# Performance work log

Measured on AMD Instinct MI355X. Metric: run time of the kernel, lower is better.

The kernel has to match this reference:

```python
import jax, jax.numpy as jnp
import numpy as np

MAX_SHIFT = 15
FREQ_WEIGHT = 0.5
EPS = 1e-8


def setup_inputs() -> dict:
    key = jax.random.key(0)
    k1, k2 = jax.random.split(key)
    preds = jax.random.normal(k1, (2048, 8192), dtype=jnp.float32)
    targets = jax.random.normal(k2, (2048, 8192), dtype=jnp.float32)
    return {"preds": preds, "targets": targets}


def reference(preds, targets):
    # ---- time-domain: best shifted Pearson correlation ----
    tc = targets - jnp.mean(targets, axis=1, keepdims=True)   # [B,T]
    std_t = jnp.sqrt(jnp.sum(tc * tc, axis=1) + EPS)          # [B]
    # rolling preserves the mean and std along the time axis, so center once
    pc = preds - jnp.mean(preds, axis=1, keepdims=True)       # [B,T]
    std_p = jnp.sqrt(jnp.sum(pc * pc, axis=1) + EPS)          # [B]

    shifts = jnp.arange(-MAX_SHIFT, MAX_SHIFT + 1)            # [31]

    def corr_at_shift(s):
        ps = jnp.roll(pc, s, axis=1)                          # [B,T]
        cov = jnp.sum(ps * tc, axis=1)                        # [B]
        return cov / (std_p * std_t)

    pearsons = jax.vmap(corr_at_shift)(shifts)                # [31,B]
    best_pearson = jnp.maximum(jnp.max(pearsons, axis=0), -1.0)
    time_loss = 1.0 - jnp.mean(best_pearson)

    # ---- frequency-domain: power-spectrum KL divergence ----
    fft_p = jnp.fft.rfft(pc, axis=1)
    fft_t = jnp.fft.rfft(tc, axis=1)
    power_p = jnp.abs(fft_p) ** 2
    power_t = jnp.abs(fft_t) ** 2
    power_p = power_p[:, 1:]   # drop DC bin
    power_t = power_t[:, 1:]
    prob_p = power_p / (jnp.sum(power_p, axis=1, keepdims=True) + EPS)
    prob_t = power_t / (jnp.sum(power_t, axis=1, keepdims=True) + EPS)
    freq_loss = jnp.sum(prob_t * (jnp.log(prob_t + EPS) - jnp.log(prob_p + EPS)), axis=1)
    freq_loss = jnp.mean(freq_loss)

    return (1.0 - FREQ_WEIGHT) * time_loss + FREQ_WEIGHT * freq_loss
```

## Files before the change

### kernel.cpp

```cpp
#include <hip/hip_runtime.h>

#define RN    8192
#define NSH   31
#define BLK   512
#define EPSF  1e-8f

__device__ __forceinline__ int SWZ(int i)  { return i ^ (((i >> 7) & 7) << 2); }
__device__ __forceinline__ int SW4(int f)  { return f ^ (((f >> 5) & 7)); }

__device__ __forceinline__ int PPOS(int k) {
  return ((k & 7) << 10) | (((k >> 3) & 7) << 7) | (((k >> 6) & 7) << 4) | (k >> 9);
}

__device__ __forceinline__ void dft8(float yr[8], float yi[8]) {
  const float C = 0.7071067811865476f;
  float ar, ai;
  float u0r = yr[0] + yr[4], u0i = yi[0] + yi[4];
  float v0r = yr[0] - yr[4], v0i = yi[0] - yi[4];
  float u1r = yr[1] + yr[5], u1i = yi[1] + yi[5];
  ar = yr[1] - yr[5]; ai = yi[1] - yi[5];
  float v1r = C * (ar + ai), v1i = C * (ai - ar);
  float u2r = yr[2] + yr[6], u2i = yi[2] + yi[6];
  ar = yr[2] - yr[6]; ai = yi[2] - yi[6];
  float v2r = ai, v2i = -ar;
  float u3r = yr[3] + yr[7], u3i = yi[3] + yi[7];
  ar = yr[3] - yr[7]; ai = yi[3] - yi[7];
  float v3r = C * (ai - ar), v3i = -C * (ar + ai);
  float t0r = u0r + u2r, t0i = u0i + u2i;
  float t1r = u1r + u3r, t1i = u1i + u3i;
  float t2r = u0r - u2r, t2i = u0i - u2i;
  float t3r = u1r - u3r, t3i = u1i - u3i;
  yr[0] = t0r + t1r; yi[0] = t0i + t1i;
  yr[4] = t0r - t1r; yi[4] = t0i - t1i;
  yr[2] = t2r + t3i; yi[2] = t2i - t3r;
  yr[6] = t2r - t3i; yi[6] = t2i + t3r;
  t0r = v0r + v2r; t0i = v0i + v2i;
  t1r = v1r + v3r; t1i = v1i + v3i;
  t2r = v0r - v2r; t2i = v0i - v2i;
  t3r = v1r - v3r; t3i = v1i - v3i;
  yr[1] = t0r + t1r; yi[1] = t0i + t1i;
  yr[5] = t0r - t1r; yi[5] = t0i - t1i;
  yr[3] = t2r + t3i; yi[3] = t2i - t3r;
  yr[7] = t2r - t3i; yi[7] = t2i + t3r;
}

__device__ __forceinline__ void dft16(float zr[16], float zi[16]) {
  float er[8], ei[8], odr[8], odi[8];
  #pragma unroll
  for (int m = 0; m < 8; ++m) {
    er[m] = zr[2*m];   ei[m] = zi[2*m];
    odr[m] = zr[2*m+1]; odi[m] = zi[2*m+1];
  }
  dft8(er, ei); dft8(odr, odi);
  const float c1 = 0.9238795325112867f, s1 = 0.3826834323650898f;
  const float C  = 0.7071067811865476f;
  const float WR[8] = {1.f,  c1,  C,  s1, 0.f, -s1, -C, -c1};
  const float WI[8] = {0.f, -s1, -C, -c1, -1.f, -c1, -C, -s1};
  #pragma unroll
  for (int q = 0; q < 8; ++q) {
    float tr = odr[q]*WR[q] - odi[q]*WI[q];
    float ti = odr[q]*WI[q] + odi[q]*WR[q];
    zr[q]     = er[q] + tr; zi[q]     = ei[q] + ti;
    zr[q + 8] = er[q] - tr; zi[q + 8] = ei[q] - ti;
  }
}

template<int LOG2S>
__device__ __forceinline__ void fft_pass8(float* zr, float* zi, int t) {
  const int S = 1 << LOG2S;
  const int g = 2 * t;
  const int j = g & (S - 1);
  const int base = ((g >> LOG2S) << (LOG2S + 3)) + j;
  float ar[8], ai[8], br[8], bi[8];
  #pragma unroll
  for (int m = 0; m < 8; ++m) {
    int i = SWZ(base + m * S);
    float2 xr = *(const float2*)&zr[i];
    float2 xim = *(const float2*)&zi[i];
    ar[m] = xr.x; br[m] = xr.y; ai[m] = xim.x; bi[m] = xim.y;
  }
  dft8(ar, ai); dft8(br, bi);
  const float angu = -3.14159265358979323846f / (4.0f * (float)S);
  float s0, c0, s1_, c1;
  __sincosf(angu * (float)j, &s0, &c0);
  __sincosf(angu * (float)(j + 1), &s1_, &c1);
  float war = c0, wai = s0, wbr = c1, wbi = s1_;
  #pragma unroll
  for (int q = 1; q < 8; ++q) {
    float tr = ar[q]*war - ai[q]*wai; ai[q] = ar[q]*wai + ai[q]*war; ar[q] = tr;
    float ur = br[q]*wbr - bi[q]*wbi; bi[q] = br[q]*wbi + bi[q]*wbr; br[q] = ur;
    if (q < 7) {
      float nr = war*c0 - wai*s0; wai = war*s0 + wai*c0; war = nr;
      float mr = wbr*c1 - wbi*s1_; wbi = wbr*s1_ + wbi*c1; wbr = mr;
    }
  }
  #pragma unroll
  for (int m = 0; m < 8; ++m) {
    int i = SWZ(base + m * S);
    *(float2*)&zr[i] = make_float2(ar[m], br[m]);
    *(float2*)&zi[i] = make_float2(ai[m], bi[m]);
  }
}

__global__ __launch_bounds__(BLK, 4) void hybrid_row_kernel(
    const float* __restrict__ preds, const float* __restrict__ targets,
    float* __restrict__ ws, int nrows)
{
  __shared__ __align__(16) float zr[RN];
  __shared__ __align__(16) float zi[RN];
  __shared__ __align__(16) float sc[2176];

  float* red  = &sc[31 * 68];
  float* covf = &sc[31 * 68 + 32];

  const int row = blockIdx.x;
  const int tid = threadIdx.x;
  const int wv  = tid >> 6;
  const int ln  = tid & 63;
  const float* __restrict__ prow = preds   + (size_t)row * RN;
  const float* __restrict__ trow = targets + (size_t)row * RN;

  float pr[16], tw[16];
  float sp = 0.f, st = 0.f;
  #pragma unroll
  for (int c = 0; c < 4; ++c) {
    int f = tid + 512 * c;
    float4 p = ((const float4*)prow)[f];
    float4 q = ((const float4*)trow)[f];
    pr[4*c+0] = p.x; pr[4*c+1] = p.y; pr[4*c+2] = p.z; pr[4*c+3] = p.w;
    tw[4*c+0] = q.x; tw[4*c+1] = q.y; tw[4*c+2] = q.z; tw[4*c+3] = q.w;
    sp += (p.x + p.y) + (p.z + p.w);
    st += (q.x + q.y) + (q.z + q.w);
  }
  #pragma unroll
  for (int off = 32; off; off >>= 1) { sp += __shfl_down(sp, off); st += __shfl_down(st, off); }
  if (ln == 0) { red[wv] = sp; red[8 + wv] = st; }
  __syncthreads();
  float mean_p = 0.f, mean_t = 0.f;
  #pragma unroll
  for (int w = 0; w < 8; ++w) { mean_p += red[w]; mean_t += red[8 + w]; }
  mean_p *= (1.0f / RN); mean_t *= (1.0f / RN);

  float ssp = 0.f, sst = 0.f;
  #pragma unroll
  for (int c = 0; c < 4; ++c) {
    int f = tid + 512 * c;
    float a0 = pr[4*c+0] - mean_p, a1 = pr[4*c+1] - mean_p;
    float a2 = pr[4*c+2] - mean_p, a3 = pr[4*c+3] - mean_p;
    float b0 = tw[4*c+0] - mean_t, b1 = tw[4*c+1] - mean_t;
    float b2 = tw[4*c+2] - mean_t, b3 = tw[4*c+3] - mean_t;
    ((float4*)zr)[SW4(f)] = make_float4(a0, a1, a2, a3);
    ((float4*)zi)[SW4(f)] = make_float4(b0, b1, b2, b3);
    ssp += (a0*a0 + a1*a1) + (a2*a2 + a3*a3);
    sst += (b0*b0 + b1*b1) + (b2*b2 + b3*b3);
  }
  #pragma unroll
  for (int off = 32; off; off >>= 1) { ssp += __shfl_down(ssp, off); sst += __shfl_down(sst, off); }
  if (ln == 0) { red[16 + wv] = ssp; red[24 + wv] = sst; }
  __syncthreads();
  float dp = 0.f, dt = 0.f;
  #pragma unroll
  for (int w = 0; w < 8; ++w) { dp += red[16 + w]; dt += red[24 + w]; }
  const float inv_denom = rsqrtf((dp + EPSF) * (dt + EPSF));

  float tq[16];
  #pragma unroll
  for (int c = 0; c < 4; ++c) {
    float4 v = ((const float4*)zi)[SW4(4 * tid + c)];
    tq[4*c+0] = v.x; tq[4*c+1] = v.y; tq[4*c+2] = v.z; tq[4*c+3] = v.w;
  }
  {
    float wa[32];
    #pragma unroll
    for (int c = 0; c < 8; ++c) {
      int f = (4 * tid - 4 + (c + 4)) & 2047;
      float4 v = ((const float4*)zr)[SW4(f)];
      wa[4*c+0] = v.x; wa[4*c+1] = v.y; wa[4*c+2] = v.z; wa[4*c+3] = v.w;
    }
    float acc[16];
    #pragma unroll
    for (int s = 0; s < 16; ++s) acc[s] = 0.f;
    #pragma unroll
    for (int e = 0; e < 16; ++e)
      #pragma unroll
      for (int s = 0; s < 16; ++s)
        acc[s] += wa[15 - s + e] * tq[e];
    #pragma unroll
    for (int s = 0; s < 16; ++s) {
      float a = acc[s];
      a += __shfl_down(a, 4); a += __shfl_down(a, 2); a += __shfl_down(a, 1);
      if ((tid & 7) == 0) sc[s * 68 + (tid >> 3)] = a;
    }
  }
  {
    float wb[32];
    #pragma unroll
    for (int c = 0; c < 8; ++c) {
      int f = (4 * tid - 4 + c) & 2047;
      float4 v = ((const float4*)zr)[SW4(f)];
      wb[4*c+0] = v.x; wb[4*c+1] = v.y; wb[4*c+2] = v.z; wb[4*c+3] = v.w;
    }
    float acc[15];
    #pragma unroll
    for (int s = 0; s < 15; ++s) acc[s] = 0.f;
    #pragma unroll
    for (int e = 0; e < 16; ++e)
      #pragma unroll
      for (int s = 0; s < 15; ++s)
        acc[s] += wb[15 - s + e] * tq[e];
    #pragma unroll
    for (int s = 0; s < 15; ++s) {
      float a = acc[s];
      a += __shfl_down(a, 4); a += __shfl_down(a, 2); a += __shfl_down(a, 1);
      if ((tid & 7) == 0) sc[(16 + s) * 68 + (tid >> 3)] = a;
    }
  }
  __syncthreads();
  if (tid < 31) {
    float a = 0.f;
    #pragma unroll
    for (int c = 0; c < 16; ++c) {
      float4 v = ((const float4*)sc)[tid * 17 + c];
      a += (v.x + v.y) + (v.z + v.w);
    }
    covf[tid] = a * inv_denom;
  }

  fft_pass8<10>(zr, zi, tid);
  __syncthreads();
  if (tid < 64) {
    float c = (tid < 31) ? covf[tid] : -3.4e38f;
    #pragma unroll
    for (int off = 32; off; off >>= 1) c = fmaxf(c, __shfl_down(c, off));
    if (tid == 0) ws[row] = fmaxf(c, -1.0f);
  }
  fft_pass8<7>(zr, zi, tid);
  __syncthreads();
  fft_pass8<4>(zr, zi, tid);
  __syncthreads();
  {
    float xr[16], xim[16];
    #pragma unroll
    for (int c = 0; c < 4; ++c) {
      float4 a = ((const float4*)zr)[SW4(4 * tid + c)];
      float4 b = ((const float4*)zi)[SW4(4 * tid + c)];
      xr[4*c+0] = a.x; xr[4*c+1] = a.y; xr[4*c+2] = a.z; xr[4*c+3] = a.w;
      xim[4*c+0] = b.x; xim[4*c+1] = b.y; xim[4*c+2] = b.z; xim[4*c+3] = b.w;
    }
    __syncthreads();
    dft16(xr, xim);
    #pragma unroll
    for (int c = 0; c < 4; ++c) {
      ((float4*)zr)[SW4(4 * tid + c)] = make_float4(xr[4*c], xr[4*c+1], xr[4*c+2], xr[4*c+3]);
      ((float4*)zi)[SW4(4 * tid + c)] = make_float4(xim[4*c], xim[4*c+1], xim[4*c+2], xim[4*c+3]);
    }
  }
  __syncthreads();

  const int l = tid & 63, wq = tid >> 6;
  float ppv[8], ttv[8];
  float Sp = 0.f, St = 0.f;
  #pragma unroll
  for (int u = 0; u < 8; ++u) {
    int j = ((l & 7) << 9) | (((l >> 3) & 7) << 6) | (u << 3) | wq;
    int k = j ? j : 4096;
    int p1 = PPOS(k), p2 = PPOS(8192 - k);
    float a = zr[SWZ(p1)], b = zi[SWZ(p1)];
    float c = zr[SWZ(p2)], d = zi[SWZ(p2)];
    float rp = a + c, ip = b - d;
    float rt = b + d, it = c - a;
    float pp = 0.25f * (rp*rp + ip*ip);
    float tt = 0.25f * (rt*rt + it*it);
    ppv[u] = pp; ttv[u] = tt; Sp += pp; St += tt;
  }
  #pragma unroll
  for (int off = 32; off; off >>= 1) { Sp += __shfl_down(Sp, off); St += __shfl_down(St, off); }
  if (ln == 0) { red[wv] = Sp; red[8 + wv] = St; }
  __syncthreads();
  float tsp = 0.f, tst = 0.f;
  #pragma unroll
  for (int w = 0; w < 8; ++w) { tsp += red[w]; tst += red[8 + w]; }
  const float inv_sp = 1.0f / (tsp + EPSF);
  const float inv_st = 1.0f / (tst + EPSF);
  float kl = 0.f;
  #pragma unroll
  for (int u = 0; u < 8; ++u) {
    float qp = ppv[u] * inv_sp;
    float qt = ttv[u] * inv_st;
    kl += qt * (__log2f(qt + EPSF) - __log2f(qp + EPSF));
  }
  kl *= 0.6931471805599453f;
  #pragma unroll
  for (int off = 32; off; off >>= 1) kl += __shfl_down(kl, off);
  if (ln == 0) red[16 + wv] = kl;
  __syncthreads();
  if (tid == 0) {
    float a = 0.f;
    #pragma unroll
    for (int w = 0; w < 8; ++w) a += red[16 + w];
    ws[nrows + row] = a;
  }
}

__global__ __launch_bounds__(256) void hybrid_final_kernel(
    const float* __restrict__ ws, float* __restrict__ out, int nrows)
{
  __shared__ float red[8];
  int tid = threadIdx.x;
  float sb = 0.f, sk = 0.f;
  for (int i = tid; i < nrows; i += 256) {
    sb += ws[i];
    sk += ws[nrows + i];
  }
  #pragma unroll
  for (int off = 32; off; off >>= 1) {
    sb += __shfl_down(sb, off);
    sk += __shfl_down(sk, off);
  }
  int wv = tid >> 6, ln = tid & 63;
  if (ln == 0) { red[wv] = sb; red[4 + wv] = sk; }
  __syncthreads();
  if (tid == 0) {
    float a = 0.f, b = 0.f;
    #pragma unroll
    for (int w = 0; w < 4; ++w) { a += red[w]; b += red[4 + w]; }
    float time_loss = 1.0f - a / (float)nrows;
    float freq_loss = b / (float)nrows;
    out[0] = 0.5f * time_loss + 0.5f * freq_loss;
  }
}

extern "C" void kernel_launch(void* const* d_in, const int* in_sizes, int n_in,
                              void* d_out, int out_size, void* d_ws, size_t ws_size,
                              hipStream_t stream) {
  const float* preds   = (const float*)d_in[0];
  const float* targets = (const float*)d_in[1];
  float* out = (float*)d_out;
  float* ws  = (float*)d_ws;
  int nrows = in_sizes[0] / RN;
  hipLaunchKernelGGL(hybrid_row_kernel, dim3(nrows), dim3(BLK), 0, stream,
                     preds, targets, ws, nrows);
  hipLaunchKernelGGL(hybrid_final_kernel, dim3(1), dim3(256), 0, stream,
                     ws, out, nrows);
}
```

Baseline: 194.7 us.

## Rework row kernel to 1024 threads with interleaved complex LDS and DPP reductions

The block size doubles to 1024 threads, so each thread now handles 8 elements and one radix-8 butterfly instead of two. Shared memory switches from split real and imaginary arrays to an interleaved float2 array with new swizzles. Shuffle-based reductions become DPP row and wave sums, and mean and variance are computed in one pass via sum and sum of squares. The separate final kernel is replaced by atomics plus a last-block-done counter, with a memset added before launch. The single-pass variance can lose precision through cancellation, and the 1024-thread blocks may lower occupancy given the register-heavy shift correlation.

```diff
diff --git a/kernel.cpp b/kernel.cpp
--- a/kernel.cpp
+++ b/kernel.cpp
@@ -2,14 +2,36 @@
 
 #define RN    8192
 #define NSH   31
-#define BLK   512
+#define BLK   1024
 #define EPSF  1e-8f
 
-__device__ __forceinline__ int SWZ(int i)  { return i ^ (((i >> 7) & 7) << 2); }
-__device__ __forceinline__ int SW4(int f)  { return f ^ (((f >> 5) & 7)); }
+__device__ __forceinline__ int SWA(int i) { return i ^ (((i >> 5) & 7) << 1); }
+__device__ __forceinline__ int SW4(int a) { return a ^ ((a >> 4) & 7); }
 
 __device__ __forceinline__ int PPOS(int k) {
   return ((k & 7) << 10) | (((k >> 3) & 7) << 7) | (((k >> 6) & 7) << 4) | (k >> 9);
+}
+
+template<int CTRL, int RMASK>
+__device__ __forceinline__ float dpp_add_f(float x) {
+  int v = __builtin_amdgcn_update_dpp(0, __float_as_int(x), CTRL, RMASK, 0xf, true);
+  return x + __int_as_float(v);
+}
+__device__ __forceinline__ float wave_sum63(float x) {
+  x = dpp_add_f<0x111, 0xf>(x);
+  x = dpp_add_f<0x112, 0xf>(x);
+  x = dpp_add_f<0x114, 0xf>(x);
+  x = dpp_add_f<0x118, 0xf>(x);
+  x = dpp_add_f<0x142, 0xa>(x);
+  x = dpp_add_f<0x143, 0xc>(x);
+  return x;
+}
+__device__ __forceinline__ float row_sum15(float x) {
+  x = dpp_add_f<0x111, 0xf>(x);
+  x = dpp_add_f<0x112, 0xf>(x);
+  x = dpp_add_f<0x114, 0xf>(x);
+  x = dpp_add_f<0x118, 0xf>(x);
+  return x;
 }
 
 __device__ __forceinline__ void dft8(float yr[8], float yi[8]) {
@@ -48,7 +70,7 @@
   float er[8], ei[8], odr[8], odi[8];
   #pragma unroll
   for (int m = 0; m < 8; ++m) {
-    er[m] = zr[2*m];   ei[m] = zi[2*m];
+    er[m] = zr[2*m];    ei[m] = zi[2*m];
     odr[m] = zr[2*m+1]; odi[m] = zi[2*m+1];
   }
   dft8(er, ei); dft8(odr, odi);
@@ -66,52 +88,40 @@
 }
 
 template<int LOG2S>
-__device__ __forceinline__ void fft_pass8(float* zr, float* zi, int t) {
+__device__ __forceinline__ void fft_pass8(float2* z, int t) {
   const int S = 1 << LOG2S;
-  const int g = 2 * t;
-  const int j = g & (S - 1);
-  const int base = ((g >> LOG2S) << (LOG2S + 3)) + j;
-  float ar[8], ai[8], br[8], bi[8];
+  const int j = t & (S - 1);
+  const int base = ((t >> LOG2S) << (LOG2S + 3)) + j;
+  float ar[8], ai[8];
   #pragma unroll
   for (int m = 0; m < 8; ++m) {
-    int i = SWZ(base + m * S);
-    float2 xr = *(const float2*)&zr[i];
-    float2 xim = *(const float2*)&zi[i];
-    ar[m] = xr.x; br[m] = xr.y; ai[m] = xim.x; bi[m] = xim.y;
-  }
-  dft8(ar, ai); dft8(br, bi);
+    float2 v = z[SWA(base + m * S)];
+    ar[m] = v.x; ai[m] = v.y;
+  }
+  dft8(ar, ai);
   const float angu = -3.14159265358979323846f / (4.0f * (float)S);
-  float s0, c0, s1_, c1;
-  __sincosf(angu * (float)j, &s0, &c0);
-  __sincosf(angu * (float)(j + 1), &s1_, &c1);
-  float war = c0, wai = s0, wbr = c1, wbi = s1_;
+  float sn, cs;
+  __sincosf(angu * (float)j, &sn, &cs);
+  float wr = cs, wi = sn;
   #pragma unroll
   for (int q = 1; q < 8; ++q) {
-    float tr = ar[q]*war - ai[q]*wai; ai[q] = ar[q]*wai + ai[q]*war; ar[q] = tr;
-    float ur = br[q]*wbr - bi[q]*wbi; bi[q] = br[q]*wbi + bi[q]*wbr; br[q] = ur;
-    if (q < 7) {
-      float nr = war*c0 - wai*s0; wai = war*s0 + wai*c0; war = nr;
-      float mr = wbr*c1 - wbi*s1_; wbi = wbr*s1_ + wbi*c1; wbr = mr;
-    }
-  }
-  #pragma unroll
-  for (int m = 0; m < 8; ++m) {
-    int i = SWZ(base + m * S);
-    *(float2*)&zr[i] = make_float2(ar[m], br[m]);
-    *(float2*)&zi[i] = make_float2(ai[m], bi[m]);
-  }
-}
-
-__global__ __launch_bounds__(BLK, 4) void hybrid_row_kernel(
+    float tr = ar[q]*wr - ai[q]*wi;
+    ai[q] = ar[q]*wi + ai[q]*wr; ar[q] = tr;
+    if (q < 7) { float nr = wr*cs - wi*sn; wi = wr*sn + wi*cs; wr = nr; }
+  }
+  #pragma unroll
+  for (int m = 0; m < 8; ++m) z[SWA(base + m * S)] = make_float2(ar[m], ai[m]);
+}
+
+__global__ __launch_bounds__(BLK, 8) void hybrid_row_kernel(
     const float* __restrict__ preds, const float* __restrict__ targets,
-    float* __restrict__ ws, int nrows)
+    float* __restrict__ wsf, float* __restrict__ out, int nrows)
 {
-  __shared__ __align__(16) float zr[RN];
-  __shared__ __align__(16) float zi[RN];
-  __shared__ __align__(16) float sc[2176];
+  __shared__ __align__(16) float2 z[RN];
+  __shared__ __align__(16) float sc[2256];
 
   float* red  = &sc[31 * 68];
-  float* covf = &sc[31 * 68 + 32];
+  float* covf = &sc[31 * 68 + 112];
 
   const int row = blockIdx.x;
   const int tid = threadIdx.x;
@@ -120,102 +130,98 @@
   const float* __restrict__ prow = preds   + (size_t)row * RN;
   const float* __restrict__ trow = targets + (size_t)row * RN;
 
-  float pr[16], tw[16];
-  float sp = 0.f, st = 0.f;
-  #pragma unroll
-  for (int c = 0; c < 4; ++c) {
-    int f = tid + 512 * c;
-    float4 p = ((const float4*)prow)[f];
-    float4 q = ((const float4*)trow)[f];
-    pr[4*c+0] = p.x; pr[4*c+1] = p.y; pr[4*c+2] = p.z; pr[4*c+3] = p.w;
-    tw[4*c+0] = q.x; tw[4*c+1] = q.y; tw[4*c+2] = q.z; tw[4*c+3] = q.w;
-    sp += (p.x + p.y) + (p.z + p.w);
-    st += (q.x + q.y) + (q.z + q.w);
-  }
-  #pragma unroll
-  for (int off = 32; off; off >>= 1) { sp += __shfl_down(sp, off); st += __shfl_down(st, off); }
-  if (ln == 0) { red[wv] = sp; red[8 + wv] = st; }
-  __syncthreads();
-  float mean_p = 0.f, mean_t = 0.f;
-  #pragma unroll
-  for (int w = 0; w < 8; ++w) { mean_p += red[w]; mean_t += red[8 + w]; }
-  mean_p *= (1.0f / RN); mean_t *= (1.0f / RN);
-
-  float ssp = 0.f, sst = 0.f;
-  #pragma unroll
-  for (int c = 0; c < 4; ++c) {
-    int f = tid + 512 * c;
-    float a0 = pr[4*c+0] - mean_p, a1 = pr[4*c+1] - mean_p;
-    float a2 = pr[4*c+2] - mean_p, a3 = pr[4*c+3] - mean_p;
-    float b0 = tw[4*c+0] - mean_t, b1 = tw[4*c+1] - mean_t;
-    float b2 = tw[4*c+2] - mean_t, b3 = tw[4*c+3] - mean_t;
-    ((float4*)zr)[SW4(f)] = make_float4(a0, a1, a2, a3);
-    ((float4*)zi)[SW4(f)] = make_float4(b0, b1, b2, b3);
-    ssp += (a0*a0 + a1*a1) + (a2*a2 + a3*a3);
-    sst += (b0*b0 + b1*b1) + (b2*b2 + b3*b3);
-  }
-  #pragma unroll
-  for (int off = 32; off; off >>= 1) { ssp += __shfl_down(ssp, off); sst += __shfl_down(sst, off); }
-  if (ln == 0) { red[16 + wv] = ssp; red[24 + wv] = sst; }
-  __syncthreads();
-  float dp = 0.f, dt = 0.f;
-  #pragma unroll
-  for (int w = 0; w < 8; ++w) { dp += red[16 + w]; dt += red[24 + w]; }
-  const float inv_denom = rsqrtf((dp + EPSF) * (dt + EPSF));
-
-  float tq[16];
-  #pragma unroll
-  for (int c = 0; c < 4; ++c) {
-    float4 v = ((const float4*)zi)[SW4(4 * tid + c)];
-    tq[4*c+0] = v.x; tq[4*c+1] = v.y; tq[4*c+2] = v.z; tq[4*c+3] = v.w;
-  }
-  {
-    float wa[32];
+  float pr[8], tw[8];
+  {
+    float4 p0 = ((const float4*)prow)[2*tid], p1 = ((const float4*)prow)[2*tid+1];
+    float4 q0 = ((const float4*)trow)[2*tid], q1 = ((const float4*)trow)[2*tid+1];
+    pr[0]=p0.x; pr[1]=p0.y; pr[2]=p0.z; pr[3]=p0.w;
+    pr[4]=p1.x; pr[5]=p1.y; pr[6]=p1.z; pr[7]=p1.w;
+    tw[0]=q0.x; tw[1]=q0.y; tw[2]=q0.z; tw[3]=q0.w;
+    tw[4]=q1.x; tw[5]=q1.y; tw[6]=q1.z; tw[7]=q1.w;
+  }
+  float sp = 0.f, st = 0.f, ssp = 0.f, sst = 0.f;
+  #pragma unroll
+  for (int e = 0; e < 8; ++e) {
+    sp += pr[e]; st += tw[e];
+    ssp += pr[e]*pr[e]; sst += tw[e]*tw[e];
+  }
+  sp = wave_sum63(sp); st = wave_sum63(st);
+  ssp = wave_sum63(ssp); sst = wave_sum63(sst);
+  if (ln == 63) { red[wv] = sp; red[16+wv] = st; red[32+wv] = ssp; red[48+wv] = sst; }
+  __syncthreads();
+  float mean_p, mean_t, inv_denom;
+  {
+    const float4* rf = (const float4*)red;
+    float a0=0.f, a1=0.f, a2=0.f, a3=0.f;
+    #pragma unroll
+    for (int c = 0; c < 4; ++c) {
+      float4 x = rf[c], y = rf[4+c], u = rf[8+c], v = rf[12+c];
+      a0 += (x.x+x.y)+(x.z+x.w); a1 += (y.x+y.y)+(y.z+y.w);
+      a2 += (u.x+u.y)+(u.z+u.w); a3 += (v.x+v.y)+(v.z+v.w);
+    }
+    mean_p = a0 * (1.0f/RN); mean_t = a1 * (1.0f/RN);
+    float dp = a2 - (float)RN * mean_p * mean_p;
+    float dt = a3 - (float)RN * mean_t * mean_t;
+    inv_denom = rsqrtf((dp + EPSF) * (dt + EPSF));
+  }
+
+  float pcr[8], tcr[8];
+  #pragma unroll
+  for (int e = 0; e < 8; ++e) { pcr[e] = pr[e] - mean_p; tcr[e] = tw[e] - mean_t; }
+  #pragma unroll
+  for (int c = 0; c < 4; ++c)
+    ((float4*)z)[SW4(4*tid + c)] =
+        make_float4(pcr[2*c], tcr[2*c], pcr[2*c+1], tcr[2*c+1]);
+  __syncthreads();
+
+  {
+    float wA[24];
+    #pragma unroll
+    for (int e = 0; e < 8; ++e) wA[e] = pcr[e];
     #pragma unroll
     for (int c = 0; c < 8; ++c) {
-      int f = (4 * tid - 4 + (c + 4)) & 2047;
-      float4 v = ((const float4*)zr)[SW4(f)];
-      wa[4*c+0] = v.x; wa[4*c+1] = v.y; wa[4*c+2] = v.z; wa[4*c+3] = v.w;
+      float4 v = ((const float4*)z)[SW4((4*tid + 4 + c) & 2047)];
+      wA[8 + 2*c] = v.x; wA[9 + 2*c] = v.z;
     }
     float acc[16];
     #pragma unroll
     for (int s = 0; s < 16; ++s) acc[s] = 0.f;
     #pragma unroll
-    for (int e = 0; e < 16; ++e)
+    for (int e = 0; e < 8; ++e)
       #pragma unroll
       for (int s = 0; s < 16; ++s)
-        acc[s] += wa[15 - s + e] * tq[e];
+        acc[s] += wA[e + 15 - s] * tcr[e];
     #pragma unroll
     for (int s = 0; s < 16; ++s) {
-      float a = acc[s];
-      a += __shfl_down(a, 4); a += __shfl_down(a, 2); a += __shfl_down(a, 1);
-      if ((tid & 7) == 0) sc[s * 68 + (tid >> 3)] = a;
-    }
-  }
-  {
-    float wb[32];
+      float a = row_sum15(acc[s]);
+      if ((tid & 15) == 15) sc[s * 68 + (tid >> 4)] = a;
+    }
+  }
+  {
+    float wB[24];
     #pragma unroll
     for (int c = 0; c < 8; ++c) {
-      int f = (4 * tid - 4 + c) & 2047;
-      float4 v = ((const float4*)zr)[SW4(f)];
-      wb[4*c+0] = v.x; wb[4*c+1] = v.y; wb[4*c+2] = v.z; wb[4*c+3] = v.w;
-    }
+      float4 v = ((const float4*)z)[SW4((4*tid - 8 + c) & 2047)];
+      wB[2*c] = v.x; wB[2*c + 1] = v.z;
+    }
+    #pragma unroll
+    for (int e = 0; e < 8; ++e) wB[16 + e] = pcr[e];
     float acc[15];
     #pragma unroll
     for (int s = 0; s < 15; ++s) acc[s] = 0.f;
     #pragma unroll
-    for (int e = 0; e < 16; ++e)
+    for (int e = 0; e < 8; ++e)
       #pragma unroll
       for (int s = 0; s < 15; ++s)
-        acc[s] += wb[15 - s + e] * tq[e];
+        acc[s] += wB[e + 15 - s] * tcr[e];
     #pragma unroll
     for (int s = 0; s < 15; ++s) {
-      float a = acc[s];
-      a += __shfl_down(a, 4); a += __shfl_down(a, 2); a += __shfl_down(a, 1);
-      if ((tid & 7) == 0) sc[(16 + s) * 68 + (tid >> 3)] = a;
-    }
-  }
-  __syncthreads();
+      float a = row_sum15(acc[s]);
+      if ((tid & 15) == 15) sc[(16 + s) * 68 + (tid >> 4)] = a;
+    }
+  }
+  __syncthreads();
+
   if (tid < 31) {
     float a = 0.f;
     #pragma unroll
@@ -225,108 +231,99 @@
     }
     covf[tid] = a * inv_denom;
   }
-
-  fft_pass8<10>(zr, zi, tid);
-  __syncthreads();
-  if (tid < 64) {
-    float c = (tid < 31) ? covf[tid] : -3.4e38f;
-    #pragma unroll
-    for (int off = 32; off; off >>= 1) c = fmaxf(c, __shfl_down(c, off));
-    if (tid == 0) ws[row] = fmaxf(c, -1.0f);
-  }
-  fft_pass8<7>(zr, zi, tid);
-  __syncthreads();
-  fft_pass8<4>(zr, zi, tid);
-  __syncthreads();
-  {
-    float xr[16], xim[16];
-    #pragma unroll
-    for (int c = 0; c < 4; ++c) {
-      float4 a = ((const float4*)zr)[SW4(4 * tid + c)];
-      float4 b = ((const float4*)zi)[SW4(4 * tid + c)];
-      xr[4*c+0] = a.x; xr[4*c+1] = a.y; xr[4*c+2] = a.z; xr[4*c+3] = a.w;
-      xim[4*c+0] = b.x; xim[4*c+1] = b.y; xim[4*c+2] = b.z; xim[4*c+3] = b.w;
-    }
-    __syncthreads();
-    dft16(xr, xim);
-    #pragma unroll
-    for (int c = 0; c < 4; ++c) {
-      ((float4*)zr)[SW4(4 * tid + c)] = make_float4(xr[4*c], xr[4*c+1], xr[4*c+2], xr[4*c+3]);
-      ((float4*)zi)[SW4(4 * tid + c)] = make_float4(xim[4*c], xim[4*c+1], xim[4*c+2], xim[4*c+3]);
-    }
-  }
-  __syncthreads();
-
-  const int l = tid & 63, wq = tid >> 6;
-  float ppv[8], ttv[8];
+  if (tid == 31) covf[31] = -3.4e38f;
+
+  fft_pass8<10>(z, tid);
+  __syncthreads();
+  if (tid == 0) {
+    const float4* cf = (const float4*)covf;
+    float m = -3.4e38f;
+    #pragma unroll
+    for (int c = 0; c < 8; ++c) {
+      float4 v = cf[c];
+      m = fmaxf(m, fmaxf(fmaxf(v.x, v.y), fmaxf(v.z, v.w)));
+    }
+    atomicAdd(&wsf[0], fmaxf(m, -1.0f));
+  }
+  fft_pass8<7>(z, tid);
+  __syncthreads();
+  fft_pass8<4>(z, tid);
+  __syncthreads();
+  if (tid < 512) {
+    float xr[16], xi[16];
+    #pragma unroll
+    for (int c = 0; c < 8; ++c) {
+      float4 v = ((const float4*)z)[SW4(8*tid + c)];
+      xr[2*c] = v.x; xi[2*c] = v.y; xr[2*c+1] = v.z; xi[2*c+1] = v.w;
+    }
+    dft16(xr, xi);
+    #pragma unroll
+    for (int c = 0; c < 8; ++c)
+      ((float4*)z)[SW4(8*tid + c)] =
+          make_float4(xr[2*c], xi[2*c], xr[2*c+1], xi[2*c+1]);
+  }
+  __syncthreads();
+
+  const int l = tid & 63, w = tid >> 6;
+  float ppv[4], ttv[4];
   float Sp = 0.f, St = 0.f;
   #pragma unroll
-  for (int u = 0; u < 8; ++u) {
-    int j = ((l & 7) << 9) | (((l >> 3) & 7) << 6) | (u << 3) | wq;
+  for (int u = 0; u < 4; ++u) {
+    int j = ((l & 7) << 9) | (((l >> 3) & 7) << 6) | (w << 2) | u;
     int k = j ? j : 4096;
-    int p1 = PPOS(k), p2 = PPOS(8192 - k);
-    float a = zr[SWZ(p1)], b = zi[SWZ(p1)];
-    float c = zr[SWZ(p2)], d = zi[SWZ(p2)];
-    float rp = a + c, ip = b - d;
-    float rt = b + d, it = c - a;
+    float2 A = z[SWA(PPOS(k))];
+    float2 B = z[SWA(PPOS(RN - k))];
+    float rp = A.x + B.x, ip = A.y - B.y;
+    float rt = A.y + B.y, it = B.x - A.x;
     float pp = 0.25f * (rp*rp + ip*ip);
     float tt = 0.25f * (rt*rt + it*it);
     ppv[u] = pp; ttv[u] = tt; Sp += pp; St += tt;
   }
-  #pragma unroll
-  for (int off = 32; off; off >>= 1) { Sp += __shfl_down(Sp, off); St += __shfl_down(St, off); }
-  if (ln == 0) { red[wv] = Sp; red[8 + wv] = St; }
-  __syncthreads();
-  float tsp = 0.f, tst = 0.f;
-  #pragma unroll
-  for (int w = 0; w < 8; ++w) { tsp += red[w]; tst += red[8 + w]; }
-  const float inv_sp = 1.0f / (tsp + EPSF);
-  const float inv_st = 1.0f / (tst + EPSF);
+  Sp = wave_sum63(Sp); St = wave_sum63(St);
+  if (ln == 63) { red[64 + wv] = Sp; red[80 + wv] = St; }
+  __syncthreads();
+  float inv_sp, inv_st;
+  {
+    const float4* rf = (const float4*)red;
+    float a0 = 0.f, a1 = 0.f;
+    #pragma unroll
+    for (int c = 0; c < 4; ++c) {
+      float4 x = rf[16 + c], y = rf[20 + c];
+      a0 += (x.x+x.y)+(x.z+x.w); a1 += (y.x+y.y)+(y.z+y.w);
+    }
+    inv_sp = 1.0f / (a0 + EPSF);
+    inv_st = 1.0f / (a1 + EPSF);
+  }
   float kl = 0.f;
   #pragma unroll
-  for (int u = 0; u < 8; ++u) {
+  for (int u = 0; u < 4; ++u) {
     float qp = ppv[u] * inv_sp;
     float qt = ttv[u] * inv_st;
     kl += qt * (__log2f(qt + EPSF) - __log2f(qp + EPSF));
   }
   kl *= 0.6931471805599453f;
-  #pragma unroll
-  for (int off = 32; off; off >>= 1) kl += __shfl_down(kl, off);
-  if (ln == 0) red[16 + wv] = kl;
-  __syncthreads();
+  kl = wave_sum63(kl);
+  if (ln == 63) red[96 + wv] = kl;
+  __syncthreads();
+
   if (tid == 0) {
+    const float4* rf = (const float4*)red;
     float a = 0.f;
     #pragma unroll
-    for (int w = 0; w < 8; ++w) a += red[16 + w];
-    ws[nrows + row] = a;
-  }
-}
-
-__global__ __launch_bounds__(256) void hybrid_final_kernel(
-    const float* __restrict__ ws, float* __restrict__ out, int nrows)
-{
-  __shared__ float red[8];
-  int tid = threadIdx.x;
-  float sb = 0.f, sk = 0.f;
-  for (int i = tid; i < nrows; i += 256) {
-    sb += ws[i];
-    sk += ws[nrows + i];
-  }
-  #pragma unroll
-  for (int off = 32; off; off >>= 1) {
-    sb += __shfl_down(sb, off);
-    sk += __shfl_down(sk, off);
-  }
-  int wv = tid >> 6, ln = tid & 63;
-  if (ln == 0) { red[wv] = sb; red[4 + wv] = sk; }
-  __syncthreads();
-  if (tid == 0) {
-    float a = 0.f, b = 0.f;
-    #pragma unroll
-    for (int w = 0; w < 4; ++w) { a += red[w]; b += red[4 + w]; }
-    float time_loss = 1.0f - a / (float)nrows;
-    float freq_loss = b / (float)nrows;
-    out[0] = 0.5f * time_loss + 0.5f * freq_loss;
+    for (int c = 0; c < 4; ++c) {
+      float4 x = rf[24 + c];
+      a += (x.x + x.y) + (x.z + x.w);
+    }
+    atomicAdd(&wsf[1], a);
+    __threadfence();
+    unsigned old = atomicAdd((unsigned*)&wsf[2], 1u);
+    if (old == (unsigned)(nrows - 1)) {
+      float sb = atomicAdd(&wsf[0], 0.0f);
+      float sk = atomicAdd(&wsf[1], 0.0f);
+      float time_loss = 1.0f - sb / (float)nrows;
+      float freq_loss = sk / (float)nrows;
+      out[0] = 0.5f * time_loss + 0.5f * freq_loss;
+    }
   }
 }
 
@@ -338,8 +335,7 @@
   float* out = (float*)d_out;
   float* ws  = (float*)d_ws;
   int nrows = in_sizes[0] / RN;
+  hipMemsetAsync(d_ws, 0, 16, stream);
   hipLaunchKernelGGL(hybrid_row_kernel, dim3(nrows), dim3(BLK), 0, stream,
-                     preds, targets, ws, nrows);
-  hipLaunchKernelGGL(hybrid_final_kernel, dim3(1), dim3(256), 0, stream,
-                     ws, out, nrows);
-}
+                     preds, targets, ws, out, nrows);
+}
```

Measured after the change: 244.9 us. 1.26x slower.
